# Performance work log

Measured on AMD Instinct MI355X. Metric: run time of the kernel, lower is better.

Reference implementation:

```python
import jax, jax.numpy as jnp
import numpy as np

B, C, N = 16, 256, 2048
D = C // 8  # q/k channel dim = 32
EPS = 1e-5
NEG_SLOPE = 0.2


def _conv1x1(x, w, b):
    # x: [B,C,N], w: [O,C], b: [O] -> [B,O,N]
    return jnp.einsum('oc,bcn->bon', w, x) + b[None, :, None]


def _bn(y, gamma, beta):
    # BatchNorm1d training-mode: per-channel stats over (batch, length)
    m = y.mean(axis=(0, 2), keepdims=True)
    v = y.var(axis=(0, 2), keepdims=True)  # biased, matches torch normalization
    return (y - m) * jax.lax.rsqrt(v + EPS) * gamma[None, :, None] + beta[None, :, None]


def setup_inputs() -> dict:
    key = jax.random.key(0)
    ks = jax.random.split(key, 14)
    s_qk = 1.0 / np.sqrt(C)
    return {
        'x': jax.random.normal(ks[0], (B, C, N), dtype=jnp.float32),
        'q_w': jax.random.normal(ks[1], (D, C), dtype=jnp.float32) * s_qk,
        'q_b': jnp.zeros((D,), jnp.float32),
        'q_g': jnp.ones((D,), jnp.float32),
        'q_be': jnp.zeros((D,), jnp.float32),
        'k_w': jax.random.normal(ks[2], (D, C), dtype=jnp.float32) * s_qk,
        'k_b': jnp.zeros((D,), jnp.float32),
        'k_g': jnp.ones((D,), jnp.float32),
        'k_be': jnp.zeros((D,), jnp.float32),
        'v_w': jax.random.normal(ks[3], (C, C), dtype=jnp.float32) * s_qk,
        'v_b': jnp.zeros((C,), jnp.float32),
        'v_g': jnp.ones((C,), jnp.float32),
        'v_be': jnp.zeros((C,), jnp.float32),
    }


def reference(x, q_w, q_b, q_g, q_be, k_w, k_b, k_g, k_be, v_w, v_b, v_g, v_be):
    # q, k: conv1x1 -> BN (no activation); v: conv1x1 -> BN -> LeakyReLU(0.2)
    q = _bn(_conv1x1(x, q_w, q_b), q_g, q_be)          # [B,D,N]
    k = _bn(_conv1x1(x, k_w, k_b), k_g, k_be)          # [B,D,N]
    v = jax.nn.leaky_relu(_bn(_conv1x1(x, v_w, v_b), v_g, v_be), NEG_SLOPE)  # [B,C,N]
    energy = jnp.einsum('bdn,bdm->bnm', q, k)          # [B,N,N]
    attn = jax.nn.softmax(energy, axis=-1)
    o = jnp.einsum('bcm,bnm->bcn', v, attn)            # attn applied over points
    return o + x
```

## Files before the change

### kernel.cpp

```cpp
#include <hip/hip_runtime.h>

#define BATCH 16
#define CH    256
#define NPT   2048
#define DQK   32
#define OTOT  320
#define EPSB  1e-5f
#define SLOPE 0.2f

typedef __attribute__((ext_vector_type(8))) short bf16x8;
typedef __attribute__((ext_vector_type(4))) float f32x4;

__device__ __forceinline__ unsigned short f2bf(float f) {
    unsigned u = __float_as_uint(f);
    u = (u + 0x7FFFu + ((u >> 16) & 1u)) >> 16;
    return (unsigned short)u;
}
__device__ __forceinline__ float bf2f(unsigned short h) {
    return __uint_as_float(((unsigned)h) << 16);
}

__global__ __launch_bounds__(256) void prep_kernel(
    const float* __restrict__ qw, const float* __restrict__ qb,
    const float* __restrict__ kw, const float* __restrict__ kb,
    const float* __restrict__ vw, const float* __restrict__ vb,
    float* __restrict__ Wt, float* __restrict__ Bv)
{
    int idx = blockIdx.x * 256 + threadIdx.x;
    int o = idx >> 8, c = idx & 255;
    float w;
    if (o < 32)      w = qw[(size_t)o * CH + c];
    else if (o < 64) w = kw[(size_t)(o - 32) * CH + c];
    else             w = vw[(size_t)(o - 64) * CH + c];
    Wt[(size_t)c * OTOT + o] = w;
    if (idx < OTOT) {
        int oo = idx;
        float bb;
        if (oo < 32)      bb = qb[oo];
        else if (oo < 64) bb = kb[oo - 32];
        else              bb = vb[oo - 64];
        Bv[oo] = bb;
    }
}

__global__ __launch_bounds__(256) void conv_kernel(
    const float* __restrict__ x,
    const float* __restrict__ Wt, const float* __restrict__ Bv,
    unsigned short* __restrict__ Ybf,
    float* __restrict__ Sum, float* __restrict__ Sq)
{
    int nh = blockIdx.x;
    int o0 = blockIdx.y * 16;
    int b  = blockIdx.z;
    int n  = nh * 1024 + threadIdx.x * 4;

    const float* xb = x + (size_t)b * CH * NPT + n;

    float4 acc[16];
#pragma unroll
    for (int j = 0; j < 16; ++j) acc[j] = make_float4(0.f, 0.f, 0.f, 0.f);

#pragma unroll 2
    for (int c = 0; c < CH; ++c) {
        float4 xv = *(const float4*)(xb + (size_t)c * NPT);
        const float* wr = Wt + (size_t)c * OTOT + o0;
#pragma unroll
        for (int j = 0; j < 16; ++j) {
            float w = wr[j];
            acc[j].x = fmaf(w, xv.x, acc[j].x);
            acc[j].y = fmaf(w, xv.y, acc[j].y);
            acc[j].z = fmaf(w, xv.z, acc[j].z);
            acc[j].w = fmaf(w, xv.w, acc[j].w);
        }
    }

    unsigned short* yb = Ybf + ((size_t)b * OTOT + o0) * NPT + n;
    int lane = threadIdx.x & 63;
#pragma unroll
    for (int j = 0; j < 16; ++j) {
        float bias = Bv[o0 + j];
        float v0 = acc[j].x + bias, v1 = acc[j].y + bias;
        float v2 = acc[j].z + bias, v3 = acc[j].w + bias;
        ushort4 o4;
        o4.x = f2bf(v0); o4.y = f2bf(v1); o4.z = f2bf(v2); o4.w = f2bf(v3);
        *(ushort4*)(yb + (size_t)j * NPT) = o4;
        float s  = v0 + v1 + v2 + v3;
        float ss = v0*v0 + v1*v1 + v2*v2 + v3*v3;
#pragma unroll
        for (int off = 32; off; off >>= 1) {
            s  += __shfl_down(s, off);
            ss += __shfl_down(ss, off);
        }
        if (lane == 0) {
            atomicAdd(&Sum[o0 + j], s);
            atomicAdd(&Sq[o0 + j], ss);
        }
    }
}

__global__ __launch_bounds__(320) void finalize_kernel(
    const float* __restrict__ Sum, const float* __restrict__ Sq,
    const float* __restrict__ qg, const float* __restrict__ qbe,
    const float* __restrict__ kg, const float* __restrict__ kbe,
    const float* __restrict__ vg, const float* __restrict__ vbe,
    float* __restrict__ A, float* __restrict__ Cc)
{
    int o = threadIdx.x;
    if (o >= OTOT) return;
    const float inv = 1.0f / (BATCH * NPT);
    float mean = Sum[o] * inv;
    float var  = Sq[o] * inv - mean * mean;
    float g, be;
    if (o < 32)      { g = qg[o];      be = qbe[o];      }
    else if (o < 64) { g = kg[o - 32]; be = kbe[o - 32]; }
    else             { g = vg[o - 64]; be = vbe[o - 64]; }
    float a = g * rsqrtf(var + EPSB);
    A[o]  = a;
    Cc[o] = be - mean * a;
}

__global__ __launch_bounds__(256) void pack_kernel(
    const unsigned short* __restrict__ Ybf,
    const float* __restrict__ A, const float* __restrict__ Cc,
    unsigned short* __restrict__ QKt, unsigned short* __restrict__ Vbf)
{
    int b = blockIdx.y, n0 = blockIdx.x * 64;
    int tid = threadIdx.x;

    for (int e = tid; e < 4096; e += 256) {
        int c = e >> 4, n4 = (e & 15) * 4;
        ushort4 v4 = *(const ushort4*)(Ybf + ((size_t)b * OTOT + 64 + c) * NPT + n0 + n4);
        float a = A[64 + c], cc = Cc[64 + c];
        ushort4 w4;
        unsigned short* pi = (unsigned short*)&v4;
        unsigned short* po = (unsigned short*)&w4;
#pragma unroll
        for (int i = 0; i < 4; ++i) {
            float y = bf2f(pi[i]) * a + cc;
            y = (y > 0.f) ? y : SLOPE * y;
            po[i] = f2bf(y);
        }
        *(ushort4*)(Vbf + ((size_t)b * CH + c) * NPT + n0 + n4) = w4;
    }

    __shared__ unsigned short T[64][72];
    for (int e = tid; e < 1024; e += 256) {
        int o = e >> 4, n4 = (e & 15) * 4;
        ushort4 v4 = *(const ushort4*)(Ybf + ((size_t)b * OTOT + o) * NPT + n0 + n4);
        float a = A[o], cc = Cc[o];
        unsigned short* pi = (unsigned short*)&v4;
#pragma unroll
        for (int i = 0; i < 4; ++i)
            T[n4 + i][o] = f2bf(bf2f(pi[i]) * a + cc);
    }
    __syncthreads();
    for (int e = tid; e < 1024; e += 256) {
        int nn = e >> 4, o4 = (e & 15) * 4;
        ushort4 v4 = *(const ushort4*)&T[nn][o4];
        *(ushort4*)(QKt + ((size_t)b * NPT + n0 + nn) * 64 + o4) = v4;
    }
}

__global__ __launch_bounds__(256, 4) void attn_kernel(
    const unsigned short* __restrict__ QKt,
    const unsigned short* __restrict__ Vbf,
    const float* __restrict__ x,
    float* __restrict__ out)
{
    int L = blockIdx.x;
    int xcd = L & 7, k = L >> 3;
    int gi = k >> 5, n0i = k & 31;
    int grp = xcd * 4 + gi;
    int b = grp >> 1, z = grp & 1;
    int n0 = n0i * 64;

    int tid = threadIdx.x;
    int w = tid >> 6, lane = tid & 63;
    int quad = lane >> 4, l16 = lane & 15;

    const unsigned short* QK = QKt + (size_t)b * NPT * 64;
    const unsigned short* V  = Vbf + ((size_t)b * CH + z * 128) * NPT;

    __shared__ unsigned short Pbf[64][72];
    __shared__ float rsw[4][64];
    __shared__ float rtot[64];

    bf16x8 qa[4];
#pragma unroll
    for (int nt = 0; nt < 4; ++nt)
        qa[nt] = *(const bf16x8*)(QK + ((size_t)(n0 + nt * 16 + l16)) * 64 + quad * 8);

    f32x4 acc[4][2];
#pragma unroll
    for (int nt = 0; nt < 4; ++nt)
#pragma unroll
        for (int ct = 0; ct < 2; ++ct)
            acc[nt][ct] = (f32x4){0.f, 0.f, 0.f, 0.f};

    float rsum[4][4];
#pragma unroll
    for (int nt = 0; nt < 4; ++nt)
#pragma unroll
        for (int r = 0; r < 4; ++r) rsum[nt][r] = 0.f;

    const f32x4 zero4 = (f32x4){0.f, 0.f, 0.f, 0.f};

    for (int mt = 0; mt < NPT / 64; ++mt) {
        bf16x8 kb = *(const bf16x8*)(QK + ((size_t)(mt * 64 + w * 16 + l16)) * 64 + 32 + quad * 8);

        __syncthreads();

#pragma unroll
        for (int nt = 0; nt < 4; ++nt) {
            f32x4 s = __builtin_amdgcn_mfma_f32_16x16x32_bf16(qa[nt], kb, zero4, 0, 0, 0);
#pragma unroll
            for (int r = 0; r < 4; ++r) {
                float p = __expf(s[r]);
                rsum[nt][r] += p;
                Pbf[nt * 16 + quad * 4 + r][w * 16 + l16] = f2bf(p);
            }
        }
        __syncthreads();

#pragma unroll
        for (int ks = 0; ks < 2; ++ks) {
            bf16x8 pa[4];
#pragma unroll
            for (int nt = 0; nt < 4; ++nt)
                pa[nt] = *(const bf16x8*)&Pbf[nt * 16 + l16][ks * 32 + quad * 8];
#pragma unroll
            for (int ct = 0; ct < 2; ++ct) {
                const unsigned short* vp =
                    V + ((size_t)(w * 32 + ct * 16 + l16)) * NPT + mt * 64 + ks * 32 + quad * 8;
                bf16x8 vb = *(const bf16x8*)vp;
#pragma unroll
                for (int nt = 0; nt < 4; ++nt)
                    acc[nt][ct] = __builtin_amdgcn_mfma_f32_16x16x32_bf16(pa[nt], vb, acc[nt][ct], 0, 0, 0);
            }
        }
    }

#pragma unroll
    for (int nt = 0; nt < 4; ++nt)
#pragma unroll
        for (int r = 0; r < 4; ++r) {
            float v = rsum[nt][r];
            v += __shfl_xor(v, 1);
            v += __shfl_xor(v, 2);
            v += __shfl_xor(v, 4);
            v += __shfl_xor(v, 8);
            if (l16 == 0) rsw[w][nt * 16 + quad * 4 + r] = v;
        }
    __syncthreads();
    if (tid < 64)
        rtot[tid] = 1.0f / (rsw[0][tid] + rsw[1][tid] + rsw[2][tid] + rsw[3][tid]);
    __syncthreads();

    float rin[4][4];
#pragma unroll
    for (int nt = 0; nt < 4; ++nt)
#pragma unroll
        for (int r = 0; r < 4; ++r) rin[nt][r] = rtot[nt * 16 + quad * 4 + r];

#pragma unroll
    for (int nt = 0; nt < 4; ++nt)
#pragma unroll
        for (int ct = 0; ct < 2; ++ct) {
            int c = z * 128 + w * 32 + ct * 16 + l16;
            int n = n0 + nt * 16 + quad * 4;
            size_t gi4 = ((size_t)b * CH + c) * NPT + n;
            float4 xv = *(const float4*)(x + gi4);
            float4 o;
            o.x = acc[nt][ct][0] * rin[nt][0] + xv.x;
            o.y = acc[nt][ct][1] * rin[nt][1] + xv.y;
            o.z = acc[nt][ct][2] * rin[nt][2] + xv.z;
            o.w = acc[nt][ct][3] * rin[nt][3] + xv.w;
            *(float4*)(out + gi4) = o;
        }
}

extern "C" void kernel_launch(void* const* d_in, const int* in_sizes, int n_in,
                              void* d_out, int out_size, void* d_ws, size_t ws_size,
                              hipStream_t stream)
{
    const float* x   = (const float*)d_in[0];
    const float* qw  = (const float*)d_in[1];
    const float* qb  = (const float*)d_in[2];
    const float* qg  = (const float*)d_in[3];
    const float* qbe = (const float*)d_in[4];
    const float* kw  = (const float*)d_in[5];
    const float* kb  = (const float*)d_in[6];
    const float* kg  = (const float*)d_in[7];
    const float* kbe = (const float*)d_in[8];
    const float* vw  = (const float*)d_in[9];
    const float* vb  = (const float*)d_in[10];
    const float* vg  = (const float*)d_in[11];
    const float* vbe = (const float*)d_in[12];
    float* out = (float*)d_out;

    unsigned short* Ybf = (unsigned short*)d_ws;
    unsigned short* QKt = Ybf + (size_t)BATCH * OTOT * NPT;
    unsigned short* Vbf = QKt + (size_t)BATCH * NPT * 64;
    float* tail = (float*)(Vbf + (size_t)BATCH * CH * NPT);
    float* Sum = tail;
    float* Sq  = tail + OTOT;
    float* A   = tail + 2 * OTOT;
    float* Cc  = tail + 3 * OTOT;
    float* Wt = (float*)QKt;
    float* Bv = Wt + (size_t)CH * OTOT;

    hipMemsetAsync(Sum, 0, 2 * OTOT * sizeof(float), stream);
    prep_kernel    <<<320, 256, 0, stream>>>(qw, qb, kw, kb, vw, vb, Wt, Bv);
    conv_kernel    <<<dim3(2, OTOT / 16, BATCH), 256, 0, stream>>>(x, Wt, Bv, Ybf, Sum, Sq);
    finalize_kernel<<<1, 320, 0, stream>>>(Sum, Sq, qg, qbe, kg, kbe, vg, vbe, A, Cc);
    pack_kernel    <<<dim3(NPT / 64, BATCH), 256, 0, stream>>>(Ybf, A, Cc, QKt, Vbf);
    attn_kernel    <<<1024, 256, 0, stream>>>(QKt, Vbf, x, out);
}
```

Baseline: 315.4 us.

## Move 1x1 conv to bf16x3 split MFMA with LDS-staged x tiles

The fp32 scalar-FMA conv kernel becomes a tiled matrix-core kernel. Weights and inputs are each split into high and low bf16 parts, and three MFMA products approximate fp32 accuracy. x tiles are converted and staged through shared memory with register prefetch of the next K slice. The goal is to move the conv GEMM off the vector ALUs, at the cost of conversion work and three times the MFMA issue count. The grid and the per-block layout are reorganised to match.

Result: faster. 276.2 us (-12.4%).

```diff
diff --git a/kernel.cpp b/kernel.cpp
--- a/kernel.cpp
+++ b/kernel.cpp
@@ -24,7 +24,8 @@
     const float* __restrict__ qw, const float* __restrict__ qb,
     const float* __restrict__ kw, const float* __restrict__ kb,
     const float* __restrict__ vw, const float* __restrict__ vb,
-    float* __restrict__ Wt, float* __restrict__ Bv)
+    unsigned short* __restrict__ Whi, unsigned short* __restrict__ Wlo,
+    float* __restrict__ Bv)
 {
     int idx = blockIdx.x * 256 + threadIdx.x;
     int o = idx >> 8, c = idx & 255;
@@ -32,7 +33,10 @@
     if (o < 32)      w = qw[(size_t)o * CH + c];
     else if (o < 64) w = kw[(size_t)(o - 32) * CH + c];
     else             w = vw[(size_t)(o - 64) * CH + c];
-    Wt[(size_t)c * OTOT + o] = w;
+    unsigned short wh = f2bf(w);
+    float rem = w - bf2f(wh);
+    Whi[idx] = wh;
+    Wlo[idx] = f2bf(rem);
     if (idx < OTOT) {
         int oo = idx;
         float bb;
@@ -45,55 +49,114 @@
 
 __global__ __launch_bounds__(256) void conv_kernel(
     const float* __restrict__ x,
-    const float* __restrict__ Wt, const float* __restrict__ Bv,
+    const unsigned short* __restrict__ Whi, const unsigned short* __restrict__ Wlo,
+    const float* __restrict__ Bv,
     unsigned short* __restrict__ Ybf,
     float* __restrict__ Sum, float* __restrict__ Sq)
 {
-    int nh = blockIdx.x;
-    int o0 = blockIdx.y * 16;
+    int ob = blockIdx.x * 64;
+    int n0 = blockIdx.y * 128;
     int b  = blockIdx.z;
-    int n  = nh * 1024 + threadIdx.x * 4;
-
-    const float* xb = x + (size_t)b * CH * NPT + n;
-
-    float4 acc[16];
-#pragma unroll
-    for (int j = 0; j < 16; ++j) acc[j] = make_float4(0.f, 0.f, 0.f, 0.f);
-
-#pragma unroll 2
-    for (int c = 0; c < CH; ++c) {
-        float4 xv = *(const float4*)(xb + (size_t)c * NPT);
-        const float* wr = Wt + (size_t)c * OTOT + o0;
-#pragma unroll
-        for (int j = 0; j < 16; ++j) {
-            float w = wr[j];
-            acc[j].x = fmaf(w, xv.x, acc[j].x);
-            acc[j].y = fmaf(w, xv.y, acc[j].y);
-            acc[j].z = fmaf(w, xv.z, acc[j].z);
-            acc[j].w = fmaf(w, xv.w, acc[j].w);
-        }
-    }
-
-    unsigned short* yb = Ybf + ((size_t)b * OTOT + o0) * NPT + n;
-    int lane = threadIdx.x & 63;
-#pragma unroll
-    for (int j = 0; j < 16; ++j) {
-        float bias = Bv[o0 + j];
-        float v0 = acc[j].x + bias, v1 = acc[j].y + bias;
-        float v2 = acc[j].z + bias, v3 = acc[j].w + bias;
-        ushort4 o4;
-        o4.x = f2bf(v0); o4.y = f2bf(v1); o4.z = f2bf(v2); o4.w = f2bf(v3);
-        *(ushort4*)(yb + (size_t)j * NPT) = o4;
-        float s  = v0 + v1 + v2 + v3;
-        float ss = v0*v0 + v1*v1 + v2*v2 + v3*v3;
-#pragma unroll
-        for (int off = 32; off; off >>= 1) {
-            s  += __shfl_down(s, off);
-            ss += __shfl_down(ss, off);
-        }
-        if (lane == 0) {
-            atomicAdd(&Sum[o0 + j], s);
-            atomicAdd(&Sq[o0 + j], ss);
+    int tid = threadIdx.x;
+    int w = tid >> 6, lane = tid & 63;
+    int quad = lane >> 4, l16 = lane & 15;
+    int wo = w >> 1, wn = w & 1;
+
+    __shared__ unsigned short Xh[128][40];
+    __shared__ unsigned short Xl[128][40];
+
+    int nl = tid & 127;
+    int ch = tid >> 7;
+    const float* xb = x + (size_t)b * CH * NPT + n0 + nl;
+
+    f32x4 acc[2][4];
+#pragma unroll
+    for (int ot = 0; ot < 2; ++ot)
+#pragma unroll
+        for (int nt = 0; nt < 4; ++nt)
+            acc[ot][nt] = (f32x4){0.f, 0.f, 0.f, 0.f};
+
+    float xv[16];
+#pragma unroll
+    for (int i = 0; i < 16; ++i)
+        xv[i] = xb[(size_t)(ch * 16 + i) * NPT];
+
+    for (int ks = 0; ks < 8; ++ks) {
+        __syncthreads();
+#pragma unroll
+        for (int g = 0; g < 4; ++g) {
+            ushort4 h4, l4;
+            unsigned short* ph = (unsigned short*)&h4;
+            unsigned short* pl = (unsigned short*)&l4;
+#pragma unroll
+            for (int j = 0; j < 4; ++j) {
+                float f = xv[g * 4 + j];
+                unsigned short h = f2bf(f);
+                ph[j] = h;
+                pl[j] = f2bf(f - bf2f(h));
+            }
+            *(ushort4*)&Xh[nl][ch * 16 + g * 4] = h4;
+            *(ushort4*)&Xl[nl][ch * 16 + g * 4] = l4;
+        }
+        __syncthreads();
+
+        if (ks < 7) {
+#pragma unroll
+            for (int i = 0; i < 16; ++i)
+                xv[i] = xb[(size_t)((ks + 1) * 32 + ch * 16 + i) * NPT];
+        }
+
+        bf16x8 ah[2], al[2];
+#pragma unroll
+        for (int ot = 0; ot < 2; ++ot) {
+            size_t orow = (size_t)(ob + wo * 32 + ot * 16 + l16) * 256 + ks * 32 + quad * 8;
+            ah[ot] = *(const bf16x8*)(Whi + orow);
+            al[ot] = *(const bf16x8*)(Wlo + orow);
+        }
+#pragma unroll
+        for (int nt = 0; nt < 4; ++nt) {
+            int nr = wn * 64 + nt * 16 + l16;
+            bf16x8 bh = *(const bf16x8*)&Xh[nr][quad * 8];
+            bf16x8 bl = *(const bf16x8*)&Xl[nr][quad * 8];
+#pragma unroll
+            for (int ot = 0; ot < 2; ++ot) {
+                acc[ot][nt] = __builtin_amdgcn_mfma_f32_16x16x32_bf16(ah[ot], bh, acc[ot][nt], 0, 0, 0);
+                acc[ot][nt] = __builtin_amdgcn_mfma_f32_16x16x32_bf16(ah[ot], bl, acc[ot][nt], 0, 0, 0);
+                acc[ot][nt] = __builtin_amdgcn_mfma_f32_16x16x32_bf16(al[ot], bh, acc[ot][nt], 0, 0, 0);
+            }
+        }
+    }
+
+#pragma unroll
+    for (int ot = 0; ot < 2; ++ot) {
+        int obase = ob + wo * 32 + ot * 16 + quad * 4;
+        float bias[4], sv[4], sq[4];
+#pragma unroll
+        for (int r = 0; r < 4; ++r) {
+            bias[r] = Bv[obase + r];
+            sv[r] = 0.f; sq[r] = 0.f;
+        }
+#pragma unroll
+        for (int nt = 0; nt < 4; ++nt) {
+            int n = n0 + wn * 64 + nt * 16 + l16;
+#pragma unroll
+            for (int r = 0; r < 4; ++r) {
+                float v = acc[ot][nt][r] + bias[r];
+                Ybf[((size_t)b * OTOT + obase + r) * NPT + n] = f2bf(v);
+                sv[r] += v; sq[r] += v * v;
+            }
+        }
+#pragma unroll
+        for (int r = 0; r < 4; ++r) {
+            float a = sv[r], q = sq[r];
+            a += __shfl_xor(a, 1); q += __shfl_xor(q, 1);
+            a += __shfl_xor(a, 2); q += __shfl_xor(q, 2);
+            a += __shfl_xor(a, 4); q += __shfl_xor(q, 4);
+            a += __shfl_xor(a, 8); q += __shfl_xor(q, 8);
+            if (l16 == 0) {
+                atomicAdd(&Sum[obase + r], a);
+                atomicAdd(&Sq[obase + r], q);
+            }
         }
     }
 }
@@ -306,12 +369,13 @@
     float* Sq  = tail + OTOT;
     float* A   = tail + 2 * OTOT;
     float* Cc  = tail + 3 * OTOT;
-    float* Wt = (float*)QKt;
-    float* Bv = Wt + (size_t)CH * OTOT;
+    unsigned short* Whi = QKt;
+    unsigned short* Wlo = Whi + (size_t)CH * OTOT;
+    float* Bv = (float*)(Wlo + (size_t)CH * OTOT);
 
     hipMemsetAsync(Sum, 0, 2 * OTOT * sizeof(float), stream);
-    prep_kernel    <<<320, 256, 0, stream>>>(qw, qb, kw, kb, vw, vb, Wt, Bv);
-    conv_kernel    <<<dim3(2, OTOT / 16, BATCH), 256, 0, stream>>>(x, Wt, Bv, Ybf, Sum, Sq);
+    prep_kernel    <<<320, 256, 0, stream>>>(qw, qb, kw, kb, vw, vb, Whi, Wlo, Bv);
+    conv_kernel    <<<dim3(5, 16, 16), 256, 0, stream>>>(x, Whi, Wlo, Bv, Ybf, Sum, Sq);
     finalize_kernel<<<1, 320, 0, stream>>>(Sum, Sq, qg, qbe, kg, kbe, vg, vbe, A, Cc);
     pack_kernel    <<<dim3(NPT / 64, BATCH), 256, 0, stream>>>(Ybf, A, Cc, QKt, Vbf);
     attn_kernel    <<<1024, 256, 0, stream>>>(QKt, Vbf, x, out);
```
